# Kernel tuning notes

Measured on AMD Instinct MI355X. Metric: run time of the kernel, lower is better.

Reference implementation:

```python
import jax, jax.numpy as jnp
import numpy as np

K, D = 512, 64
B, H, W = 32, 64, 64


def setup_inputs() -> dict:
    key = jax.random.key(0)
    k1, k2 = jax.random.split(key)
    z_e_x = jax.random.normal(k1, (B, D, H, W), dtype=jnp.float32)
    # nn.Embedding weight initialized uniform(-1/K, 1/K)
    codebook = jax.random.uniform(k2, (K, D), dtype=jnp.float32,
                                  minval=-1.0 / K, maxval=1.0 / K)
    return {"z_e_x": z_e_x, "codebook": codebook}


def _quantize_indices(flat, codebook):
    # distances[n,k] = ||c_k||^2 + ||x_n||^2 - 2 x_n . c_k  (addmm form)
    cb_sqr = jnp.sum(codebook * codebook, axis=1)            # [K]
    x_sqr = jnp.sum(flat * flat, axis=1, keepdims=True)      # [N,1]
    distances = cb_sqr + x_sqr - 2.0 * (flat @ codebook.T)   # [N,K]
    return jnp.argmin(distances, axis=1)                     # [N]


def reference(z_e_x, codebook):
    # VQEmbedding.straight_through forward: returns (z_q_x, z_q_x_bar), both NCHW.
    b, d, h, w = z_e_x.shape
    x = jnp.transpose(z_e_x, (0, 2, 3, 1))       # NHWC
    flat = x.reshape(-1, d)                      # [N,D]
    idx = _quantize_indices(flat, codebook)      # [N]
    codes = jnp.take(codebook, idx, axis=0).reshape(b, h, w, d)
    z_q = jnp.transpose(codes, (0, 3, 1, 2))     # NCHW
    # z_q_x (detached codebook path) and z_q_x_bar (live codebook path) are
    # numerically identical in the forward pass.
    return (z_q, z_q)
```

## Files before the change

kernel.cpp:

```cpp
#include <hip/hip_runtime.h>


typedef short bf16x8 __attribute__((ext_vector_type(8)));
typedef float f32x4  __attribute__((ext_vector_type(4)));

#define KCODES 512
#define DDIM 64
#define HWSZ 4096
#define NPOS 131072
#define POSB 128
#define NBLK (NPOS / POSB)
#define OUT2_OFF 8388608
#define S_X 132
#define S_X4 (S_X / 4)

#define GLD_LDS16(gsrc, ldst)                                                   \
    __builtin_amdgcn_global_load_lds(                                           \
        (const __attribute__((address_space(1))) void*)(gsrc),                  \
        (__attribute__((address_space(3))) void*)(ldst), 16, 0, 0)

__device__ __forceinline__ unsigned short f2bf_rne(float f) {
    unsigned u = __builtin_bit_cast(unsigned, f);
    unsigned r = u + 0x7FFFu + ((u >> 16) & 1u);
    return (unsigned short)(r >> 16);
}
__device__ __forceinline__ float bf2f(unsigned short h) {
    unsigned u = ((unsigned)h) << 16;
    return __builtin_bit_cast(float, u);
}

__device__ __forceinline__ float np_sumsq64(const float* __restrict__ a) {
#pragma clang fp contract(off)
    float r0 = a[0]*a[0], r1 = a[1]*a[1], r2 = a[2]*a[2], r3 = a[3]*a[3];
    float r4 = a[4]*a[4], r5 = a[5]*a[5], r6 = a[6]*a[6], r7 = a[7]*a[7];
#pragma unroll
    for (int i = 8; i < 64; i += 8) {
        r0 += a[i+0]*a[i+0]; r1 += a[i+1]*a[i+1];
        r2 += a[i+2]*a[i+2]; r3 += a[i+3]*a[i+3];
        r4 += a[i+4]*a[i+4]; r5 += a[i+5]*a[i+5];
        r6 += a[i+6]*a[i+6]; r7 += a[i+7]*a[i+7];
    }
    return ((r0+r1)+(r2+r3)) + ((r4+r5)+(r6+r7));
}

__global__ __launch_bounds__(256) void vq_prep(
    const float* __restrict__ cb, unsigned short* __restrict__ wsb,
    float* __restrict__ wscb)
{
    if (blockIdx.x < 128) {
        int u = blockIdx.x * 256 + threadIdx.x;
        int k = u >> 6, d = u & 63;
        float c = cb[u];
        unsigned short ch = f2bf_rne(c);
        float clf = c - bf2f(ch);
        unsigned short cl = f2bf_rne(clf);
        int tile = k >> 4, n = k & 15;
        int chunk = d >> 5, quad = (d >> 3) & 3, j = d & 7;
        int lane = quad * 16 + n;
        size_t base = ((((size_t)tile*2 + chunk)*2 + 0)*64 + lane)*8 + j;
        wsb[base]       = (unsigned short)ch;
        wsb[base + 512] = (unsigned short)cl;
    } else {
        int k = (blockIdx.x - 128) * 256 + threadIdx.x;
        if (k < KCODES) wscb[k] = np_sumsq64(cb + k * DDIM);
    }
}

__global__ __launch_bounds__(256, 4) void vq_main(
    const float* __restrict__ z, const float* __restrict__ cb,
    const unsigned short* __restrict__ wsb, const float* __restrict__ wscb,
    float* __restrict__ out)
{
#pragma clang fp contract(off)
    __shared__ float4 s_xbuf4[DDIM * S_X4];
    __shared__ float s_cbsqr[KCODES];
    __shared__ float s_xsqr[POSB];
    __shared__ float s_part[2 * POSB];
    __shared__ int   s_idx[POSB];
    __shared__ int   s_flist[POSB];
    __shared__ int   s_cnt;
    float* s_regA = (float*)s_xbuf4;

    const int tid = threadIdx.x;
    const int wv = tid >> 6, ln = tid & 63;
    const int m = ln & 15, q = ln >> 4;
    const int n0 = blockIdx.x * POSB;
    const long gbase = (long)(n0 >> 12) * (DDIM * HWSZ) + (n0 & 4095);

    if (tid == 0) s_cnt = 0;
    s_cbsqr[tid] = wscb[tid];
    s_cbsqr[tid + 256] = wscb[tid + 256];

    {
        const float4* z4 = (const float4*)(z + gbase);
#pragma unroll
        for (int i = 0; i < 8; ++i) {
            int v = i * 256 + tid;
            int d = v >> 5, p4 = v & 31;
            s_xbuf4[d * S_X4 + p4] = z4[d * (HWSZ / 4) + p4];
        }
    }
    __syncthreads();

    {
        int p = tid & 127, h = tid >> 7;
        float r0 = 0.f, r1 = 0.f, r2 = 0.f, r3 = 0.f;
#pragma unroll
        for (int i = 0; i < 8; ++i) {
            float a0 = s_regA[(8*i + 4*h + 0) * S_X + p];
            float a1 = s_regA[(8*i + 4*h + 1) * S_X + p];
            float a2 = s_regA[(8*i + 4*h + 2) * S_X + p];
            float a3 = s_regA[(8*i + 4*h + 3) * S_X + p];
            r0 += a0*a0; r1 += a1*a1; r2 += a2*a2; r3 += a3*a3;
        }
        s_part[h * POSB + p] = (r0 + r1) + (r2 + r3);
    }

    bf16x8 Ah[4], Al[4];
#pragma unroll
    for (int rt = 0; rt < 2; ++rt)
#pragma unroll
        for (int c = 0; c < 2; ++c) {
            int pos = wv * 32 + rt * 16 + m;
            bf16x8 ah, al;
#pragma unroll
            for (int j = 0; j < 8; ++j) {
                float xv = s_regA[(c*32 + q*8 + j) * S_X + pos];
                unsigned short hh = f2bf_rne(xv);
                float lo = xv - bf2f(hh);
                ah[j] = (short)hh;
                al[j] = (short)f2bf_rne(lo);
            }
            Ah[rt*2 + c] = ah; Al[rt*2 + c] = al;
        }
    __syncthreads();

    char* const stg0 = (char*)s_regA;
    char* const stg1 = (char*)s_regA + 16384;
    {
        const unsigned short* src = wsb + (0 * 4 + wv) * 2048 + ln * 8;
        char* dst = stg0 + wv * 4096;
#pragma unroll
        for (int i = 0; i < 4; ++i) GLD_LDS16(src + i * 512, dst + i * 1024);
    }
    if (tid < POSB) s_xsqr[tid] = s_part[tid] + s_part[POSB + tid];
    asm volatile("s_waitcnt vmcnt(0)" ::: "memory");
    __syncthreads();

    float m1[8], m2[8]; int t1[8];
#pragma unroll
    for (int i = 0; i < 8; ++i) { m1[i] = 3.4e38f; m2[i] = 3.4e38f; t1[i] = 0; }

    {
        char* cur = stg0;
        char* nxt = stg1;
        for (int g = 0; g < 8; ++g) {
            if (g < 7) {
                const unsigned short* src = wsb + ((g + 1) * 4 + wv) * 2048 + ln * 8;
                char* dst = nxt + wv * 4096;
#pragma unroll
                for (int i = 0; i < 4; ++i) GLD_LDS16(src + i * 512, dst + i * 1024);
            }
            const unsigned short* sb = (const unsigned short*)cur;
#pragma unroll
            for (int ti = 0; ti < 4; ++ti) {
                int t = g * 4 + ti;
                const unsigned short* s = sb + ti * 2048 + ln * 8;
                bf16x8 Bh0 = *(const bf16x8*)(s);
                bf16x8 Bl0 = *(const bf16x8*)(s + 512);
                bf16x8 Bh1 = *(const bf16x8*)(s + 1024);
                bf16x8 Bl1 = *(const bf16x8*)(s + 1536);
                float cbv = s_cbsqr[t * 16 + m];
#pragma unroll
                for (int rt = 0; rt < 2; ++rt) {
                    f32x4 acc = {0.f, 0.f, 0.f, 0.f};
                    acc = __builtin_amdgcn_mfma_f32_16x16x32_bf16(Al[rt*2+0], Bh0, acc, 0,0,0);
                    acc = __builtin_amdgcn_mfma_f32_16x16x32_bf16(Ah[rt*2+0], Bl0, acc, 0,0,0);
                    acc = __builtin_amdgcn_mfma_f32_16x16x32_bf16(Ah[rt*2+0], Bh0, acc, 0,0,0);
                    acc = __builtin_amdgcn_mfma_f32_16x16x32_bf16(Al[rt*2+1], Bh1, acc, 0,0,0);
                    acc = __builtin_amdgcn_mfma_f32_16x16x32_bf16(Ah[rt*2+1], Bl1, acc, 0,0,0);
                    acc = __builtin_amdgcn_mfma_f32_16x16x32_bf16(Ah[rt*2+1], Bh1, acc, 0,0,0);
#pragma unroll
                    for (int r = 0; r < 4; ++r) {
                        float sc = fmaf(-2.f, acc[r], cbv);
                        int cell = rt * 4 + r;
                        bool lt = sc < m1[cell];
                        m2[cell] = fminf(m2[cell], lt ? m1[cell] : sc);
                        if (lt) { m1[cell] = sc; t1[cell] = t; }
                    }
                }
            }
            asm volatile("s_waitcnt vmcnt(0)" ::: "memory");
            __syncthreads();
            char* tmp = cur; cur = nxt; nxt = tmp;
        }
    }

#pragma unroll
    for (int cell = 0; cell < 8; ++cell) {
        int rt = cell >> 2, r = cell & 3;
        float v1 = m1[cell], v2 = m2[cell];
        int i1 = t1[cell] * 16 + m;
#pragma unroll
        for (int s = 1; s < 16; s <<= 1) {
            float o1 = __shfl_xor(v1, s);
            float o2 = __shfl_xor(v2, s);
            int   oi = __shfl_xor(i1, s);
            bool take = (o1 < v1) || (o1 == v1 && oi < i1);
            float lose = take ? v1 : o1;
            if (take) { v1 = o1; i1 = oi; }
            v2 = fminf(fminf(v2, o2), lose);
        }
        if (m == 0) {
            int pos = wv * 32 + rt * 16 + q * 4 + r;
            float xs = s_xsqr[pos];
            float sx = 8.0f * sqrtf(xs) * 1.01f;
            float amax = 0.00196f * sx + 0.01f;
            float eps = 1.5f * (3.0f * 1.52587890625e-5f * 0.00196f * sx
                                + 500.f * 5.96e-8f * amax);
            float delta = 2.4e-7f * (xs + 1.0f) + 64.f * 1.2e-7f * amax;
            float W = 2.f * eps + 2.f * delta + 1e-9f;
            int flag = (v2 - v1 <= W) ? (1 << 30) : 0;
            s_idx[pos] = i1 | flag;
        }
    }
    __syncthreads();
    if (tid < POSB) {
        if (s_idx[tid] & (1 << 30)) {
            int slot = atomicAdd(&s_cnt, 1);
            s_flist[slot] = tid;
        }
    }
    __syncthreads();

    const int cnt = s_cnt;
    for (int i = wv; i < cnt; i += 4) {
        int p = __builtin_amdgcn_readfirstlane(s_flist[i]);
        float xv = z[gbase + (long)ln * HWSZ + p];
        float xs = s_xsqr[p];
        float dot[8];
#pragma unroll
        for (int j = 0; j < 8; ++j) dot[j] = 0.f;
        const float* crow = cb + (ln * 8) * DDIM;
        for (int dc = 0; dc < 16; ++dc) {
            float x0 = __shfl(xv, dc*4 + 0);
            float x1 = __shfl(xv, dc*4 + 1);
            float x2 = __shfl(xv, dc*4 + 2);
            float x3 = __shfl(xv, dc*4 + 3);
#pragma unroll
            for (int j = 0; j < 8; ++j) {
                float4 cv = *(const float4*)(crow + j * DDIM + dc * 4);
                dot[j] = fmaf(x0, cv.x, dot[j]);
                dot[j] = fmaf(x1, cv.y, dot[j]);
                dot[j] = fmaf(x2, cv.z, dot[j]);
                dot[j] = fmaf(x3, cv.w, dot[j]);
            }
        }
        float bv = 3.4e38f; int bi = 0;
#pragma unroll
        for (int j = 0; j < 8; ++j) {
            int k = ln * 8 + j;
            float tt = s_cbsqr[k] + xs;
            float e = fmaf(-2.f, dot[j], tt);
            if (e < bv) { bv = e; bi = k; }
        }
#pragma unroll
        for (int s = 1; s < 64; s <<= 1) {
            float ov = __shfl_xor(bv, s); int oi = __shfl_xor(bi, s);
            if (ov < bv || (ov == bv && oi < bi)) { bv = ov; bi = oi; }
        }
        if (ln == 0) s_idx[p] = bi;
    }
    __syncthreads();

    {
        int p = tid & 127, hf = tid >> 7;
        int idx = s_idx[p] & 0x3FFFFFFF;
        const float4* crow4 = (const float4*)(cb + idx * DDIM + hf * 32);
#pragma unroll
        for (int j4 = 0; j4 < 8; ++j4) {
            float4 cv = crow4[j4];
            int d = hf * 32 + j4 * 4;
            s_regA[(d + 0) * S_X + p] = cv.x;
            s_regA[(d + 1) * S_X + p] = cv.y;
            s_regA[(d + 2) * S_X + p] = cv.z;
            s_regA[(d + 3) * S_X + p] = cv.w;
        }
    }
    __syncthreads();

    {
        float4* o4 = (float4*)(out + gbase);
#pragma unroll
        for (int i = 0; i < 8; ++i) {
            int v = i * 256 + tid;
            int d = v >> 5, p4 = v & 31;
            float4 val = s_xbuf4[d * S_X4 + p4];
            size_t off = (size_t)d * (HWSZ / 4) + p4;
            o4[off] = val;
            o4[off + (OUT2_OFF / 4)] = val;
        }
    }
}

extern "C" void kernel_launch(void* const* d_in, const int* in_sizes, int n_in,
                              void* d_out, int out_size, void* d_ws, size_t ws_size,
                              hipStream_t stream) {
    const float* z  = (const float*)d_in[0];
    const float* cb = (const float*)d_in[1];
    float* out = (float*)d_out;
    unsigned short* wsb = (unsigned short*)d_ws;
    float* wscb = (float*)((char*)d_ws + 131072);
    vq_prep<<<130, 256, 0, stream>>>(cb, wsb, wscb);
    vq_main<<<NBLK, 256, 0, stream>>>(z, cb, wsb, wscb, out);
}
```

Measured before the change: 151.2 us.

## Replace double-buffered codebook staging with single buffer and interleave MFMA chains

Removes the double-buffered LDS prefetch of codebook tiles. Each group is now loaded into one buffer, waited on, computed, then synchronized again. The MFMA accumulation is also reordered so the two row-tile accumulators interleave, and B fragments are loaded in two halves to reduce live registers. This likely lowers register pressure and LDS footprint, but it gives up the overlap of global loads with compute and adds a barrier per group.

After: 150.1 us. Within noise of the previous version (-0.7%).

```diff
diff --git a/kernel.cpp b/kernel.cpp
--- a/kernel.cpp
+++ b/kernel.cpp
@@ -134,65 +134,63 @@
             Ah[rt*2 + c] = ah; Al[rt*2 + c] = al;
         }
     __syncthreads();
-
-    char* const stg0 = (char*)s_regA;
-    char* const stg1 = (char*)s_regA + 16384;
-    {
-        const unsigned short* src = wsb + (0 * 4 + wv) * 2048 + ln * 8;
-        char* dst = stg0 + wv * 4096;
-#pragma unroll
-        for (int i = 0; i < 4; ++i) GLD_LDS16(src + i * 512, dst + i * 1024);
-    }
     if (tid < POSB) s_xsqr[tid] = s_part[tid] + s_part[POSB + tid];
-    asm volatile("s_waitcnt vmcnt(0)" ::: "memory");
-    __syncthreads();
 
     float m1[8], m2[8]; int t1[8];
 #pragma unroll
     for (int i = 0; i < 8; ++i) { m1[i] = 3.4e38f; m2[i] = 3.4e38f; t1[i] = 0; }
 
     {
-        char* cur = stg0;
-        char* nxt = stg1;
+        char* const stg = (char*)s_regA;
         for (int g = 0; g < 8; ++g) {
-            if (g < 7) {
-                const unsigned short* src = wsb + ((g + 1) * 4 + wv) * 2048 + ln * 8;
-                char* dst = nxt + wv * 4096;
+            {
+                const unsigned short* src = wsb + (g * 4 + wv) * 2048 + ln * 8;
+                char* dst = stg + wv * 4096;
 #pragma unroll
                 for (int i = 0; i < 4; ++i) GLD_LDS16(src + i * 512, dst + i * 1024);
-            }
-            const unsigned short* sb = (const unsigned short*)cur;
-#pragma unroll
-            for (int ti = 0; ti < 4; ++ti) {
-                int t = g * 4 + ti;
-                const unsigned short* s = sb + ti * 2048 + ln * 8;
-                bf16x8 Bh0 = *(const bf16x8*)(s);
-                bf16x8 Bl0 = *(const bf16x8*)(s + 512);
-                bf16x8 Bh1 = *(const bf16x8*)(s + 1024);
-                bf16x8 Bl1 = *(const bf16x8*)(s + 1536);
-                float cbv = s_cbsqr[t * 16 + m];
-#pragma unroll
-                for (int rt = 0; rt < 2; ++rt) {
-                    f32x4 acc = {0.f, 0.f, 0.f, 0.f};
-                    acc = __builtin_amdgcn_mfma_f32_16x16x32_bf16(Al[rt*2+0], Bh0, acc, 0,0,0);
-                    acc = __builtin_amdgcn_mfma_f32_16x16x32_bf16(Ah[rt*2+0], Bl0, acc, 0,0,0);
-                    acc = __builtin_amdgcn_mfma_f32_16x16x32_bf16(Ah[rt*2+0], Bh0, acc, 0,0,0);
-                    acc = __builtin_amdgcn_mfma_f32_16x16x32_bf16(Al[rt*2+1], Bh1, acc, 0,0,0);
-                    acc = __builtin_amdgcn_mfma_f32_16x16x32_bf16(Ah[rt*2+1], Bl1, acc, 0,0,0);
-                    acc = __builtin_amdgcn_mfma_f32_16x16x32_bf16(Ah[rt*2+1], Bh1, acc, 0,0,0);
-#pragma unroll
-                    for (int r = 0; r < 4; ++r) {
-                        float sc = fmaf(-2.f, acc[r], cbv);
-                        int cell = rt * 4 + r;
-                        bool lt = sc < m1[cell];
-                        m2[cell] = fminf(m2[cell], lt ? m1[cell] : sc);
-                        if (lt) { m1[cell] = sc; t1[cell] = t; }
-                    }
-                }
             }
             asm volatile("s_waitcnt vmcnt(0)" ::: "memory");
             __syncthreads();
-            char* tmp = cur; cur = nxt; nxt = tmp;
+#pragma unroll
+            for (int ti = 0; ti < 4; ++ti) {
+                int t = g * 4 + ti;
+                const unsigned short* sB = (const unsigned short*)(stg + ti * 4096) + ln * 8;
+                float cbv = s_cbsqr[t * 16 + m];
+                f32x4 acc0 = {0.f, 0.f, 0.f, 0.f};
+                f32x4 acc1 = {0.f, 0.f, 0.f, 0.f};
+                bf16x8 Bh = *(const bf16x8*)(sB);
+                bf16x8 Bl = *(const bf16x8*)(sB + 512);
+                acc0 = __builtin_amdgcn_mfma_f32_16x16x32_bf16(Al[0], Bh, acc0, 0,0,0);
+                acc0 = __builtin_amdgcn_mfma_f32_16x16x32_bf16(Ah[0], Bl, acc0, 0,0,0);
+                acc0 = __builtin_amdgcn_mfma_f32_16x16x32_bf16(Ah[0], Bh, acc0, 0,0,0);
+                acc1 = __builtin_amdgcn_mfma_f32_16x16x32_bf16(Al[2], Bh, acc1, 0,0,0);
+                acc1 = __builtin_amdgcn_mfma_f32_16x16x32_bf16(Ah[2], Bl, acc1, 0,0,0);
+                acc1 = __builtin_amdgcn_mfma_f32_16x16x32_bf16(Ah[2], Bh, acc1, 0,0,0);
+                Bh = *(const bf16x8*)(sB + 1024);
+                Bl = *(const bf16x8*)(sB + 1536);
+                acc0 = __builtin_amdgcn_mfma_f32_16x16x32_bf16(Al[1], Bh, acc0, 0,0,0);
+                acc0 = __builtin_amdgcn_mfma_f32_16x16x32_bf16(Ah[1], Bl, acc0, 0,0,0);
+                acc0 = __builtin_amdgcn_mfma_f32_16x16x32_bf16(Ah[1], Bh, acc0, 0,0,0);
+                acc1 = __builtin_amdgcn_mfma_f32_16x16x32_bf16(Al[3], Bh, acc1, 0,0,0);
+                acc1 = __builtin_amdgcn_mfma_f32_16x16x32_bf16(Ah[3], Bl, acc1, 0,0,0);
+                acc1 = __builtin_amdgcn_mfma_f32_16x16x32_bf16(Ah[3], Bh, acc1, 0,0,0);
+#pragma unroll
+                for (int r = 0; r < 4; ++r) {
+                    float sc = fmaf(-2.f, acc0[r], cbv);
+                    bool lt = sc < m1[r];
+                    m2[r] = fminf(m2[r], lt ? m1[r] : sc);
+                    if (lt) { m1[r] = sc; t1[r] = t; }
+                }
+#pragma unroll
+                for (int r = 0; r < 4; ++r) {
+                    float sc = fmaf(-2.f, acc1[r], cbv);
+                    int cell = 4 + r;
+                    bool lt = sc < m1[cell];
+                    m2[cell] = fminf(m2[cell], lt ? m1[cell] : sc);
+                    if (lt) { m1[cell] = sc; t1[cell] = t; }
+                }
+            }
+            __syncthreads();
         }
     }
 
```
